# Optimization experiments

Hardware: AMD Instinct MI355X
Metric: run time of the kernel (lower is better)

Reference implementation:

```python
import jax, jax.numpy as jnp
import numpy as np
from jax import lax

B, N, G, K, D = 16, 8192, 512, 32, 128
MLP = [128, 128, 256]
EPS = 1e-5


def setup_inputs() -> dict:
    key = jax.random.key(0)
    ks = jax.random.split(key, 2 + len(MLP))
    inp = {
        "xyz": jax.random.normal(ks[0], (B, N, 3), jnp.float32),
        "points": jax.random.normal(ks[1], (B, N, D), jnp.float32),
    }
    last = D
    for li, oc in enumerate(MLP, 1):
        inp[f"W{li}"] = jax.random.normal(ks[1 + li], (oc, last), jnp.float32) / np.float32(np.sqrt(last))
        inp[f"b{li}"] = jnp.zeros((oc,), jnp.float32)
        inp[f"g{li}"] = jnp.ones((oc,), jnp.float32)
        inp[f"be{li}"] = jnp.zeros((oc,), jnp.float32)
        last = oc
    return inp


def _fps(xyz, num_group):
    # farthest point sampling, deterministic start at index 0 -> idx [B, G]
    b, n, _ = xyz.shape
    init_idx = jnp.zeros((b,), jnp.int32)

    def step(carry, _):
        dists, last_idx = carry                                   # [B,N], [B]
        last = jnp.take_along_axis(xyz, last_idx[:, None, None], axis=1)  # [B,1,3]
        d = jnp.sum((xyz - last) ** 2, axis=-1)                   # [B,N]
        dists = jnp.minimum(dists, d)
        nxt = jnp.argmax(dists, axis=1).astype(jnp.int32)
        return (dists, nxt), nxt

    init = (jnp.full((b, n), 1e10, jnp.float32), init_idx)
    _, rest = lax.scan(step, init, None, length=num_group - 1)    # [G-1, B]
    return jnp.concatenate([init_idx[None, :], rest], axis=0).T   # [B, G]


def _forward(xyz, points, layers):
    b = xyz.shape[0]
    center_idx = _fps(xyz, G)                                       # [B,G]
    center = jnp.take_along_axis(xyz, center_idx[:, :, None], axis=1)  # [B,G,3]
    # KNN: pairwise squared distances center->points, top-k smallest
    d2 = (jnp.sum(center ** 2, -1)[:, :, None]
          + jnp.sum(xyz ** 2, -1)[:, None, :]
          - 2.0 * jnp.einsum("bgc,bnc->bgn", center, xyz))          # [B,G,N]
    _, idx = lax.top_k(-d2, K)                                      # [B,G,K]
    feats = jnp.take_along_axis(points, idx.reshape(b, G * K, 1), axis=1)
    feats = feats.reshape(b, G, K, -1)                              # [B,G,K,D]
    x = feats.transpose(0, 3, 2, 1)                                 # [B,D,K,G]
    for (W, bb, g, be) in layers:
        x = jnp.einsum("oc,bckg->bokg", W, x) + bb[None, :, None, None]
        m = jnp.mean(x, axis=(0, 2, 3), keepdims=True)
        v = jnp.var(x, axis=(0, 2, 3), keepdims=True)               # biased, as torch BN
        x = (x - m) * lax.rsqrt(v + EPS) * g[None, :, None, None] + be[None, :, None, None]
        x = jax.nn.relu(x)
    new_points = jnp.max(x, axis=2).transpose(0, 2, 1)              # [B,G,C_out]
    return center, new_points


def reference(xyz, points, W1, b1, g1, be1, W2, b2, g2, be2, W3, b3, g3, be3):
    layers = [(W1, b1, g1, be1), (W2, b2, g2, be2), (W3, b3, g3, be3)]
    return _forward(xyz, points, layers)
```

## Files before the change

kernel.cpp:

```cpp
#include <hip/hip_runtime.h>
#include <hip/hip_bf16.h>

#define BB 16
#define NN 8192
#define GG 512
#define KK 32
#define DD 128

typedef __attribute__((ext_vector_type(8))) short bf16x8;
typedef __attribute__((ext_vector_type(4))) float f32x4;
typedef __attribute__((ext_vector_type(2))) float f32x2;
typedef __attribute__((ext_vector_type(2))) unsigned int u32x2;
typedef __attribute__((ext_vector_type(4))) unsigned int u32x4;
typedef __attribute__((ext_vector_type(2))) unsigned long long u64x2;

__device__ __forceinline__ unsigned short f2bf(float f){
  unsigned int u = __builtin_bit_cast(unsigned int, f);
  unsigned int r = (u + 0x7FFFu + ((u >> 16) & 1u)) >> 16;
  return (unsigned short)r;
}
__device__ __forceinline__ float bf2f(unsigned short h){
  unsigned int u = ((unsigned int)h) << 16;
  return __builtin_bit_cast(float, u);
}
// ... 110 lines not shown
#undef RESCAN2
      bv = gmin[0]; bi = gidx[0];
#pragma unroll
      for (int gi = 1; gi < 8; ++gi)
        if (gmin[gi] < bv){ bv = gmin[gi]; bi = gidx[gi]; }
    }
  }

  if (lane < KK) wlist[w][lane] = mykey;
  __syncthreads();
  if (lane < KK){
    unsigned long long K = mykey;
    const unsigned long long* other = wlist[1 - w];
    int cnt = 0;
#pragma unroll
    for (int j = 0; j < KK; ++j) cnt += (other[j] < K) ? 1 : 0;
    int rank = lane + cnt;
    if (rank < KK) outidx[rank] = (int)(unsigned int)K;
  }
  __syncthreads();
  if (t128 < KK) kidx[(size_t)bg*KK + t128] = outidx[t128];
}

__global__ __launch_bounds__(1024)
void fps_a_kernel(const float* __restrict__ xyz, const float* __restrict__ points,
                  const float* __restrict__ W1, const float* __restrict__ W2,
                  const float* __restrict__ W3,
                  float* __restrict__ center_out, float* __restrict__ ddws,
                  float* __restrict__ xs, float* __restrict__ ys,
                  float* __restrict__ zs, float* __restrict__ pps,
                  unsigned short* __restrict__ Wbf,
                  unsigned short* __restrict__ pointsbf)
{
#pragma clang fp contract(off)
  __shared__ unsigned long long slot[3][2] __attribute__((aligned(16)));
  __shared__ float tbl[NN][4] __attribute__((aligned(16)));
  __shared__ float outbuf[GG][4] __attribute__((aligned(16)));
  int t = threadIdx.x;
  if (blockIdx.x >= BB){
    int pb = blockIdx.x - BB;
    size_t i = ((size_t)pb*1024 + t)*8;
    f32x4 u0 = *(const f32x4*)(points + i);
    f32x4 u1 = *(const f32x4*)(points + i + 4);
    unsigned int w0 = f2bf(u0[0]) | ((unsigned int)f2bf(u0[1]) << 16);
    unsigned int w1 = f2bf(u0[2]) | ((unsigned int)f2bf(u0[3]) << 16);
    unsigned int w2 = f2bf(u1[0]) | ((unsigned int)f2bf(u1[1]) << 16);
    unsigned int w3 = f2bf(u1[2]) | ((unsigned int)f2bf(u1[3]) << 16);
    u32x4 pv = {w0, w1, w2, w3};
    *(u32x4*)(pointsbf + i) = pv;
    if (pb < 128){
      int n = pb*1024 + t;
      float x = xyz[(size_t)n*3 + 0];
      float y = xyz[(size_t)n*3 + 1];
      float z = xyz[(size_t)n*3 + 2];
      xs[n] = x; ys[n] = y; zs[n] = z;
      pps[n] = (x*x + y*y) + z*z;
    }
    if (pb < 64){
      int n = pb*1024 + t;
      float v;
      if (n < 16384)      v = W1[n];
      else if (n < 32768) v = W2[n - 16384];
      else                v = W3[n - 32768];
      Wbf[n] = f2bf(v);
    }
    return;
  }
  int b = blockIdx.x;
  int lane = t & 63, wid = t >> 6;
  const float* base = xyz + (size_t)b * NN * 3;
  f32x2 px[4], py[4], pz[4], dd[4];
#pragma unroll
  for (int i = 0; i < 4; ++i){
    int n0 = i*2048 + t, n1 = n0 + 1024;
    float x0 = base[n0*3+0], y0 = base[n0*3+1], z0 = base[n0*3+2];
    float x1 = base[n1*3+0], y1 = base[n1*3+1], z1 = base[n1*3+2];
    px[i] = (f32x2){x0, x1}; py[i] = (f32x2){y0, y1}; pz[i] = (f32x2){z0, z1};
    dd[i] = (f32x2){1e10f, 1e10f};
    f32x4 c0 = {x0, y0, z0, 0.f}, c1 = {x1, y1, z1, 0.f};
    *(f32x4*)&tbl[n0][0] = c0;
    *(f32x4*)&tbl[n1][0] = c1;
  }
  float lx = base[0], ly = base[1], lz = base[2];
  if (t < 6) slot[t >> 1][t & 1] = 0;
  if (t == 0){
    f32x4 ob = {lx, ly, lz, 0.f};
    *(f32x4*)&outbuf[0][0] = ob;
  }
  __syncthreads();
  for (int g = 1; g < 256; ++g){
    f32x2 lxv = (f32x2){lx, lx}, lyv = (f32x2){ly, ly}, lzv = (f32x2){lz, lz};
    f32x2 vm = (f32x2){-1.f, -1.f};
#pragma unroll
    for (int i = 0; i < 4; ++i){
      f32x2 dx = px[i] - lxv, dy = py[i] - lyv, dz = pz[i] - lzv;
      f32x2 s = (dx*dx + dy*dy) + dz*dz;
      f32x2 nd = __builtin_elementwise_min(dd[i], s);
      dd[i] = nd;
      vm = __builtin_elementwise_max(vm, nd);
    }
    float m = fmaxf(vm.x, vm.y);
    int mi = 0x7FFFFFFF;
#pragma unroll
    for (int i = 3; i >= 0; --i){
      int n0 = i*2048 + t;
      if (dd[i].y == m) mi = n0 + 1024;
      if (dd[i].x == m) mi = n0;
    }
    float wmax = wave_max_f32(m);
    bool cnd = (m == wmax);
    unsigned long long mask = __ballot(cnd);
    int n_wave;
    if (__popcll(mask) == 1){
      n_wave = __builtin_amdgcn_readlane(mi, (int)__builtin_ctzll(mask));
    } else {
      int cand = cnd ? mi : 0x7FFFFFFF;
      n_wave = wave_min_i32(cand);
    }
    unsigned long long key =
        ((unsigned long long)__builtin_bit_cast(unsigned int, wmax) << 32)
      | (unsigned int)(~n_wave);
    int p = g - (g/3)*3;
    if (lane == 0) atomicMax(&slot[p][wid & 1], key);
    __syncthreads();
    u64x2 sA = *(const u64x2*)&slot[p][0];
    unsigned long long M = sA.x > sA.y ? sA.x : sA.y;
    int n_win = (int)~((unsigned int)M);
    f32x4 cw = *(const f32x4*)&tbl[n_win][0];
    lx = cw[0]; ly = cw[1]; lz = cw[2];
    if (t == 0) *(f32x4*)&outbuf[g][0] = cw;
    if (t < 2){
      int z = p + 2; if (z >= 3) z -= 3;
      slot[z][t] = 0;
    }
  }
  __syncthreads();
  if (t < 256){
    center_out[((size_t)b*GG + t)*3 + 0] = outbuf[t][0];
    center_out[((size_t)b*GG + t)*3 + 1] = outbuf[t][1];
    center_out[((size_t)b*GG + t)*3 + 2] = outbuf[t][2];
  }
  f32x4 s0 = {dd[0].x, dd[0].y, dd[1].x, dd[1].y};
  f32x4 s1 = {dd[2].x, dd[2].y, dd[3].x, dd[3].y};
  float* dp = ddws + ((size_t)b*1024 + t)*8;
  *(f32x4*)dp       = s0;
  *(f32x4*)(dp + 4) = s1;
}

__global__ __launch_bounds__(1024)
void fps_b_kernel(const float* __restrict__ xyz, float* __restrict__ center_out,
                  const float* __restrict__ ddws,
                  const float* __restrict__ xs, const float* __restrict__ ys,
                  const float* __restrict__ zs, const float* __restrict__ pps,
                  int* __restrict__ kidx)
{
#pragma clang fp contract(off)
  __shared__ unsigned long long slot[3][2] __attribute__((aligned(16)));
  __shared__ float tbl[NN][4] __attribute__((aligned(16)));
  __shared__ float outbuf[GG][4] __attribute__((aligned(16)));
  __shared__ unsigned long long kwl[8][2][KK] __attribute__((aligned(16)));
  __shared__ int kout[8][KK];
  int t = threadIdx.x;
  if (blockIdx.x >= BB){
    int pb = blockIdx.x - BB;
    int sub = t >> 7, t128 = t & 127;
    int idx = pb*8 + sub;
    int b = idx >> 8, g = idx & 255;
    knn_group(b*GG + g, t128, xs, ys, zs, pps, center_out, kidx,
              kwl[sub], kout[sub]);
    return;
  }
  int b = blockIdx.x;
  int lane = t & 63, wid = t >> 6;
  const float* base = xyz + (size_t)b * NN * 3;
  f32x2 px[4], py[4], pz[4], dd[4];
  const float* dp = ddws + ((size_t)b*1024 + t)*8;
  f32x4 s0 = *(const f32x4*)dp;
  f32x4 s1 = *(const f32x4*)(dp + 4);
  dd[0] = (f32x2){s0[0], s0[1]};
  dd[1] = (f32x2){s0[2], s0[3]};
  dd[2] = (f32x2){s1[0], s1[1]};
  dd[3] = (f32x2){s1[2], s1[3]};
#pragma unroll
  for (int i = 0; i < 4; ++i){
    int n0 = i*2048 + t, n1 = n0 + 1024;
    float x0 = base[n0*3+0], y0 = base[n0*3+1], z0 = base[n0*3+2];
    float x1 = base[n1*3+0], y1 = base[n1*3+1], z1 = base[n1*3+2];
    px[i] = (f32x2){x0, x1}; py[i] = (f32x2){y0, y1}; pz[i] = (f32x2){z0, z1};
    f32x4 c0 = {x0, y0, z0, 0.f}, c1 = {x1, y1, z1, 0.f};
    *(f32x4*)&tbl[n0][0] = c0;
    *(f32x4*)&tbl[n1][0] = c1;
  }
  float lx = center_out[((size_t)b*GG + 255)*3 + 0];
  float ly = center_out[((size_t)b*GG + 255)*3 + 1];
  float lz = center_out[((size_t)b*GG + 255)*3 + 2];
  if (t < 6) slot[t >> 1][t & 1] = 0;
  __syncthreads();
  for (int g = 256; g < GG; ++g){
    f32x2 lxv = (f32x2){lx, lx}, lyv = (f32x2){ly, ly}, lzv = (f32x2){lz, lz};
    f32x2 vm = (f32x2){-1.f, -1.f};
#pragma unroll
    for (int i = 0; i < 4; ++i){
      f32x2 dx = px[i] - lxv, dy = py[i] - lyv, dz = pz[i] - lzv;
      f32x2 s = (dx*dx + dy*dy) + dz*dz;
      f32x2 nd = __builtin_elementwise_min(dd[i], s);
      dd[i] = nd;
      vm = __builtin_elementwise_max(vm, nd);
    }
    float m = fmaxf(vm.x, vm.y);
    int mi = 0x7FFFFFFF;
#pragma unroll
    for (int i = 3; i >= 0; --i){
      int n0 = i*2048 + t;
      if (dd[i].y == m) mi = n0 + 1024;
      if (dd[i].x == m) mi = n0;
    }
    float wmax = wave_max_f32(m);
    bool cnd = (m == wmax);
    unsigned long long mask = __ballot(cnd);
    int n_wave;
    if (__popcll(mask) == 1){
      n_wave = __builtin_amdgcn_readlane(mi, (int)__builtin_ctzll(mask));
    } else {
      int cand = cnd ? mi : 0x7FFFFFFF;
      n_wave = wave_min_i32(cand);
    }
    unsigned long long key =
        ((unsigned long long)__builtin_bit_cast(unsigned int, wmax) << 32)
      | (unsigned int)(~n_wave);
    int p = g - (g/3)*3;
    if (lane == 0) atomicMax(&slot[p][wid & 1], key);
    __syncthreads();
    u64x2 sA = *(const u64x2*)&slot[p][0];
    unsigned long long M = sA.x > sA.y ? sA.x : sA.y;
    int n_win = (int)~((unsigned int)M);
    f32x4 cw = *(const f32x4*)&tbl[n_win][0];
    lx = cw[0]; ly = cw[1]; lz = cw[2];
    if (t == 0) *(f32x4*)&outbuf[g][0] = cw;
    if (t < 2){
      int z = p + 2; if (z >= 3) z -= 3;
      slot[z][t] = 0;
    }
  }
  __syncthreads();
  if (t < 256){
    int g = 256 + t;
    center_out[((size_t)b*GG + g)*3 + 0] = outbuf[g][0];
    center_out[((size_t)b*GG + g)*3 + 1] = outbuf[g][1];
    center_out[((size_t)b*GG + g)*3 + 2] = outbuf[g][2];
  }
}

template<int OC, int MODE, bool STATS, bool STORE, bool POOL>
__device__ __forceinline__ void gemm_body(int sbid, int t, int slot,
    const unsigned short* __restrict__ Wbf, const float* __restrict__ bias,
    const unsigned short* __restrict__ pointsbf, const int* __restrict__ kidx,
    const unsigned short* __restrict__ Xin,
    const float* __restrict__ psum_in, const float* __restrict__ gin,
    const float* __restrict__ bein,
    unsigned short* __restrict__ Yout, float* __restrict__ psum,
    float* __restrict__ rawmax, float* __restrict__ rawmin,
    unsigned short* smem, float* ssc, float* ssh)
{
  constexpr int MF = OC / 64;
  int l = t & 63, w = t >> 6;
  int l15 = l & 15, lh = l >> 4;
  int jbase = sbid * 64;
  int obase = w * (OC / 4);

  if constexpr (MODE == 1){
    if (t < 128){
      float s = 0.f, q = 0.f;
#pragma unroll
      for (int sl = 0; sl < 64; ++sl){
        s += psum_in[sl*128 + t];
        q += psum_in[64*128 + sl*128 + t];
      }
      const float inv = 1.f / 262144.f;
      float mean = s * inv;
      float var  = q * inv - mean*mean;
      float sc = gin[t] * rsqrtf(var + 1e-5f);
      ssc[t] = sc;
      ssh[t] = bein[t] - mean*sc;
    }
  }

  bf16x8 a[MF][4];
#pragma unroll
  for (int m = 0; m < MF; ++m)
#pragma unroll
    for (int kf = 0; kf < 4; ++kf){
      int row = obase + m*16 + l15;
      int c8  = kf*32 + lh*8;
      a[m][kf] = *(const bf16x8*)(Wbf + (size_t)row*128 + c8);
    }

  if constexpr (MODE == 1) __syncthreads();

#pragma unroll
  for (int q = 0; q < 4; ++q){
    int ci = q*256 + t;
    int j = ci >> 4, cc = ci & 15;
    unsigned short* dst = &smem[j*128 + ((cc ^ (j & 15)) * 8)];
    if constexpr (MODE == 0){
      int jg = jbase + j;
      int bb = jg >> 14;
      int row = kidx[jg];
      const unsigned short* src = pointsbf + ((size_t)bb*NN + row)*DD + cc*8;
      *(u32x4*)dst = *(const u32x4*)src;
    } else {
      const unsigned short* src = Xin + ((size_t)(jbase + j))*128 + cc*8;
      u32x4 v = *(const u32x4*)src;
      int c0 = cc * 8;
      unsigned int wo[4];
#pragma unroll
      for (int p = 0; p < 4; ++p){
        float x0 = bf2f((unsigned short)(v[p] & 0xFFFFu));
        float x1 = bf2f((unsigned short)(v[p] >> 16));
        x0 = fmaxf(fmaf(x0, ssc[c0 + 2*p],     ssh[c0 + 2*p]),     0.f);
        x1 = fmaxf(fmaf(x1, ssc[c0 + 2*p + 1], ssh[c0 + 2*p + 1]), 0.f);
        wo[p] = f2bf(x0) | ((unsigned int)f2bf(x1) << 16);
      }
      u32x4 pv = {wo[0], wo[1], wo[2], wo[3]};
      *(u32x4*)dst = pv;
    }
  }
  __syncthreads();

  f32x4 acc[MF][4];
#pragma unroll
  for (int m = 0; m < MF; ++m)
#pragma unroll
    for (int n = 0; n < 4; ++n)
      acc[m][n] = (f32x4){0.f, 0.f, 0.f, 0.f};

#pragma unroll
  for (int n = 0; n < 4; ++n){
    bf16x8 bfr[4];
    int j = n*16 + l15;
#pragma unroll
    for (int kf = 0; kf < 4; ++kf){
      int ch = kf*4 + lh;
      bfr[kf] = *(const bf16x8*)&smem[j*128 + ((ch ^ (j & 15)) * 8)];
    }
#pragma unroll
    for (int m = 0; m < MF; ++m)
#pragma unroll
      for (int kf = 0; kf < 4; ++kf)
        acc[m][n] = __builtin_amdgcn_mfma_f32_16x16x32_bf16(a[m][kf], bfr[kf], acc[m][n], 0, 0, 0);
  }

#pragma unroll
  for (int m = 0; m < MF; ++m){
    int o0 = obase + m*16 + lh*4;
    f32x4 bv = *(const f32x4*)(bias + o0);
#pragma unroll
    for (int n = 0; n < 4; ++n) acc[m][n] += bv;
  }

  if constexpr (STATS){
#pragma unroll
    for (int m = 0; m < MF; ++m){
#pragma unroll
      for (int r = 0; r < 4; ++r){
        float s = 0.f, q2 = 0.f;
#pragma unroll
        for (int n = 0; n < 4; ++n){ float v = acc[m][n][r]; s += v; q2 += v*v; }
        s  += __shfl_xor(s, 1);  s  += __shfl_xor(s, 2);  s  += __shfl_xor(s, 4);  s  += __shfl_xor(s, 8);
        q2 += __shfl_xor(q2, 1); q2 += __shfl_xor(q2, 2); q2 += __shfl_xor(q2, 4); q2 += __shfl_xor(q2, 8);
        if (l15 == 0){
          int o = obase + m*16 + lh*4 + r;
          atomicAdd(psum + slot*OC + o, s);
          atomicAdd(psum + 64*OC + slot*OC + o, q2);
        }
      }
    }
  }

  if constexpr (POOL){
#pragma unroll
    for (int m = 0; m < MF; ++m){
      int o0 = obase + m*16 + lh*4;
      f32x4 gmx0, gmx1, gmn0, gmn1;
#pragma unroll
      for (int r = 0; r < 4; ++r){
        float v0 = acc[m][0][r], v1 = acc[m][1][r];
        float v2 = acc[m][2][r], v3 = acc[m][3][r];
        float ax0 = fmaxf(v0, v1), ax1 = fmaxf(v2, v3);
        float an0 = fminf(v0, v1), an1 = fminf(v2, v3);
#pragma unroll
        for (int mk = 1; mk < 16; mk <<= 1){
          ax0 = fmaxf(ax0, __shfl_xor(ax0, mk));
          ax1 = fmaxf(ax1, __shfl_xor(ax1, mk));
          an0 = fminf(an0, __shfl_xor(an0, mk));
          an1 = fminf(an1, __shfl_xor(an1, mk));
        }
        gmx0[r] = ax0; gmx1[r] = ax1; gmn0[r] = an0; gmn1[r] = an1;
      }
      if (l15 == 0){
        int gg = jbase >> 5;
        *(f32x4*)(rawmax + (size_t)gg*256 + o0)       = gmx0;
        *(f32x4*)(rawmax + (size_t)(gg + 1)*256 + o0) = gmx1;
        *(f32x4*)(rawmin + (size_t)gg*256 + o0)       = gmn0;
        *(f32x4*)(rawmin + (size_t)(gg + 1)*256 + o0) = gmn1;
      }
    }
  }

  if constexpr (STORE){
    __syncthreads();
#pragma unroll
    for (int m = 0; m < MF; ++m){
      int o0 = obase + m*16 + lh*4;
      int co = o0 >> 2;
#pragma unroll
      for (int n = 0; n < 4; ++n){
        int j = n*16 + l15;
        unsigned int w0 = f2bf(acc[m][n][0]) | ((unsigned int)f2bf(acc[m][n][1]) << 16);
        unsigned int w1 = f2bf(acc[m][n][2]) | ((unsigned int)f2bf(acc[m][n][3]) << 16);
        u32x2 pv = {w0, w1};
        *(u32x2*)&smem[j*OC + ((co ^ ((j & 15) << 1)) * 4)] = pv;
      }
    }
    __syncthreads();
    constexpr int CPR = OC / 4;
    constexpr int CPT = (64 * CPR) / 256;
#pragma unroll
    for (int q = 0; q < CPT; ++q){
      int ci = q*256 + t;
      int j = ci / CPR, co = ci % CPR;
      u32x2 v = *(const u32x2*)&smem[j*OC + ((co ^ ((j & 15) << 1)) * 4)];
      *(u32x2*)(Yout + (size_t)(jbase + j)*OC + co*4) = v;
    }
  }
}

__global__ __launch_bounds__(256)
void knn_gemm1_kernel(const float* __restrict__ xs, const float* __restrict__ ys,
                      const float* __restrict__ zs, const float* __restrict__ pps,
                      const float* __restrict__ center, int* __restrict__ kidx,
                      const unsigned short* __restrict__ Wbf,
                      const float* __restrict__ b1,
                      const unsigned short* __restrict__ pointsbf,
                      unsigned short* __restrict__ Y1, float* __restrict__ psumA)
{
  __shared__ unsigned short smem[64 * 128];
  __shared__ unsigned long long kwl[2][2][KK] __attribute__((aligned(16)));
  __shared__ int kout[2][KK];
  int bid = blockIdx.x, t = threadIdx.x;
  if (bid < 2048){
    int swz = (bid & 7) * 256 + (bid >> 3);
    int sub = t >> 7, t128 = t & 127;
    int idx = swz*2 + sub;
    int b = idx >> 8, g = 256 + (idx & 255);
    knn_group(b*GG + g, t128, xs, ys, zs, pps, center, kidx,
              kwl[sub], kout[sub]);
    return;
  }
  int h = bid - 2048;
  int hs = (h & 7) * 256 + (h >> 3);
  int sbid = (hs >> 7) * 256 + (hs & 127);
  gemm_body<128, 0, true, true, false>(sbid, t, bid & 63,
      Wbf, b1, pointsbf, kidx, nullptr, nullptr, nullptr, nullptr,
      Y1, psumA, nullptr, nullptr, smem, nullptr, nullptr);
}

template<int OC, int MODE, bool STATS, bool STORE, bool POOL>
__global__ __launch_bounds__(256)
void gemm_kernel(int gridmode,
                 const unsigned short* __restrict__ Wbf, const float* __restrict__ bias,
                 const unsigned short* __restrict__ pointsbf, const int* __restrict__ kidx,
                 const unsigned short* __restrict__ Xin,
                 const float* __restrict__ psum_in, const float* __restrict__ gin,
                 const float* __restrict__ bein,
                 unsigned short* __restrict__ Yout, float* __restrict__ psum,
                 float* __restrict__ rawmax, float* __restrict__ rawmin)
{
  __shared__ unsigned short smem[64 * OC];
  __shared__ float ssc[128], ssh[128];
  int bid = blockIdx.x, t = threadIdx.x;
  int sbid;
  if (gridmode == 0){
    sbid = (bid & 7) * 512 + (bid >> 3);
  } else {
    int hs = (bid & 7) * 256 + (bid >> 3);
    sbid = (hs >> 7) * 256 + 128 + (hs & 127);
  }
  gemm_body<OC, MODE, STATS, STORE, POOL>(sbid, t, bid & 63,
      Wbf, bias, pointsbf, kidx, Xin, psum_in, gin, bein,
      Yout, psum, rawmax, rawmin, smem, ssc, ssh);
}

__global__ __launch_bounds__(256)
void finish3_kernel(const float* __restrict__ psumC, const float* __restrict__ g3,
                    const float* __restrict__ be3, const float* __restrict__ rawmax,
                    const float* __restrict__ rawmin, float* __restrict__ opool)
{
  __shared__ float ssc[256], ssh[256];
  int t = threadIdx.x;
  {
    float s = 0.f, q = 0.f;
#pragma unroll
    for (int sl = 0; sl < 64; ++sl){
      s += psumC[sl*256 + t];
      q += psumC[64*256 + sl*256 + t];
    }
    const float inv = 1.f / 262144.f;
    float mean = s * inv;
    float var  = q * inv - mean*mean;
    float sc = g3[t] * rsqrtf(var + 1e-5f);
    ssc[t] = sc;
    ssh[t] = be3[t] - mean*sc;
// ... 37 lines not shown
  auto alloc = [&](size_t bytes) -> void* {
    void* p = ws + off;
    off += (bytes + 255) & ~(size_t)255;
    return p;
  };
  unsigned short* Y1   = (unsigned short*)alloc((size_t)262144*128*2);
  unsigned short* Y2   = (unsigned short*)alloc((size_t)262144*128*2);
  int*   kidx = (int*)  alloc((size_t)262144*4);
  unsigned short* Wbf = (unsigned short*)alloc((size_t)65536*2);
  float* rawmax = (float*)alloc((size_t)8192*256*4);
  float* rawmin = (float*)alloc((size_t)8192*256*4);
  float* psumA = (float*)alloc((size_t)2*64*128*4);
  float* psumB = (float*)alloc((size_t)2*64*128*4);
  float* psumC = (float*)alloc((size_t)2*64*256*4);
  float* xsb  = (float*)alloc((size_t)131072*4);
  float* ysb  = (float*)alloc((size_t)131072*4);
  float* zsb  = (float*)alloc((size_t)131072*4);
  float* ppsb = (float*)alloc((size_t)131072*4);
  float* ddws = (float*)alloc((size_t)16*1024*8*4);
  unsigned short* pointsbf = Y2;

  hipMemsetAsync(psumA, 0, (size_t)(2*64*128 + 2*64*128 + 2*64*256)*4 + 1024, stream);

  fps_a_kernel<<<BB + 2048, 1024, 0, stream>>>(
      xyz, points, W1, W2, W3, center, ddws, xsb, ysb, zsb, ppsb, Wbf, pointsbf);
  fps_b_kernel<<<BB + 512, 1024, 0, stream>>>(
      xyz, center, ddws, xsb, ysb, zsb, ppsb, kidx);

  knn_gemm1_kernel<<<4096, 256, 0, stream>>>(
      xsb, ysb, zsb, ppsb, center, kidx, Wbf, b1, pointsbf, Y1, psumA);

  gemm_kernel<128, 0, true, true, false><<<2048, 256, 0, stream>>>(
      2, Wbf, b1, pointsbf, kidx, nullptr, nullptr, nullptr, nullptr,
      Y1, psumA, nullptr, nullptr);

  gemm_kernel<128, 1, true, true, false><<<4096, 256, 0, stream>>>(
      0, Wbf + 16384, b2, nullptr, nullptr, Y1, psumA, g1, be1,
      Y2, psumB, nullptr, nullptr);

  gemm_kernel<256, 1, true, false, true><<<4096, 256, 0, stream>>>(
      0, Wbf + 32768, b3, nullptr, nullptr, Y2, psumB, g2, be2,
      nullptr, psumC, rawmax, rawmin);

  finish3_kernel<<<512, 256, 0, stream>>>(psumC, g3, be3, rawmax, rawmin, opool);
}
```

Baseline: 779.3 us.

## Split FPS into four phases and overlap KNN and GEMM1 with each phase

The serial farthest-point-sampling loop is now split into four launches of 128 centers each instead of two of 256. Filler blocks in each launch run KNN for the centers from the previous phase and layer-1 GEMM tiles for centers from two phases back. The aim is to hide more of the latency-bound FPS chain behind independent work and shrink the tail kernels. In exchange it adds two kernel launches and reloads the point coordinates and distance state for each phase. Co-resident filler blocks may also contend with the FPS blocks for CU resources.

```diff
diff --git a/kernel.cpp b/kernel.cpp
--- a/kernel.cpp
+++ b/kernel.cpp
@@ -156,22 +156,327 @@
   if (t128 < KK) kidx[(size_t)bg*KK + t128] = outidx[t128];
 }
 
+__device__ __forceinline__ void fps_part(const float* __restrict__ xyz,
+    float* __restrict__ center_out, float* __restrict__ ddws,
+    int b, int t, int g0, int g1, bool save_dd, char* lds)
+{
+#pragma clang fp contract(off)
+  float (*tbl)[4]    = (float(*)[4])lds;
+  float (*outbuf)[4] = (float(*)[4])(lds + 131072);
+  unsigned long long (*slot)[2] =
+      (unsigned long long(*)[2])(lds + 131072 + 2048);
+  int lane = t & 63, wid = t >> 6;
+  const float* base = xyz + (size_t)b * NN * 3;
+  f32x2 px[4], py[4], pz[4], dd[4];
+  if (g0 == 1){
+#pragma unroll
+    for (int i = 0; i < 4; ++i) dd[i] = (f32x2){1e10f, 1e10f};
+  } else {
+    const float* dp = ddws + ((size_t)b*1024 + t)*8;
+    f32x4 s0 = *(const f32x4*)dp;
+    f32x4 s1 = *(const f32x4*)(dp + 4);
+    dd[0] = (f32x2){s0[0], s0[1]};
+    dd[1] = (f32x2){s0[2], s0[3]};
+    dd[2] = (f32x2){s1[0], s1[1]};
+    dd[3] = (f32x2){s1[2], s1[3]};
+  }
+#pragma unroll
+  for (int i = 0; i < 4; ++i){
+    int n0 = i*2048 + t, n1 = n0 + 1024;
+    float x0 = base[n0*3+0], y0 = base[n0*3+1], z0 = base[n0*3+2];
+    float x1 = base[n1*3+0], y1 = base[n1*3+1], z1 = base[n1*3+2];
+    px[i] = (f32x2){x0, x1}; py[i] = (f32x2){y0, y1}; pz[i] = (f32x2){z0, z1};
+    f32x4 c0 = {x0, y0, z0, 0.f}, c1 = {x1, y1, z1, 0.f};
+    *(f32x4*)&tbl[n0][0] = c0;
+    *(f32x4*)&tbl[n1][0] = c1;
+  }
+  float lx, ly, lz;
+  if (g0 == 1){ lx = base[0]; ly = base[1]; lz = base[2]; }
+  else {
+    lx = center_out[((size_t)b*GG + g0 - 1)*3 + 0];
+    ly = center_out[((size_t)b*GG + g0 - 1)*3 + 1];
+    lz = center_out[((size_t)b*GG + g0 - 1)*3 + 2];
+  }
+  if (t < 6) slot[t >> 1][t & 1] = 0;
+  __syncthreads();
+  for (int g = g0; g < g1; ++g){
+    f32x2 lxv = (f32x2){lx, lx}, lyv = (f32x2){ly, ly}, lzv = (f32x2){lz, lz};
+    f32x2 vm = (f32x2){-1.f, -1.f};
+#pragma unroll
+    for (int i = 0; i < 4; ++i){
+      f32x2 dx = px[i] - lxv, dy = py[i] - lyv, dz = pz[i] - lzv;
+      f32x2 s = (dx*dx + dy*dy) + dz*dz;
+      f32x2 nd = __builtin_elementwise_min(dd[i], s);
+      dd[i] = nd;
+      vm = __builtin_elementwise_max(vm, nd);
+    }
+    float m = fmaxf(vm.x, vm.y);
+    int mi = 0x7FFFFFFF;
+#pragma unroll
+    for (int i = 3; i >= 0; --i){
+      int n0 = i*2048 + t;
+      if (dd[i].y == m) mi = n0 + 1024;
+      if (dd[i].x == m) mi = n0;
+    }
+    float wmax = wave_max_f32(m);
+    bool cnd = (m == wmax);
+    unsigned long long mask = __ballot(cnd);
+    int n_wave;
+    if (__popcll(mask) == 1){
+      n_wave = __builtin_amdgcn_readlane(mi, (int)__builtin_ctzll(mask));
+    } else {
+      int cand = cnd ? mi : 0x7FFFFFFF;
+      n_wave = wave_min_i32(cand);
+    }
+    unsigned long long key =
+        ((unsigned long long)__builtin_bit_cast(unsigned int, wmax) << 32)
+      | (unsigned int)(~n_wave);
+    int p = g - (g/3)*3;
+    if (lane == 0) atomicMax(&slot[p][wid & 1], key);
+    __syncthreads();
+    u64x2 sA = *(const u64x2*)&slot[p][0];
+    unsigned long long M = sA.x > sA.y ? sA.x : sA.y;
+    int n_win = (int)~((unsigned int)M);
+    f32x4 cw = *(const f32x4*)&tbl[n_win][0];
+    lx = cw[0]; ly = cw[1]; lz = cw[2];
+    if (t == 0) *(f32x4*)&outbuf[g - g0][0] = cw;
+    if (t < 2){
+      int z = p + 2; if (z >= 3) z -= 3;
+      slot[z][t] = 0;
+    }
+  }
+  __syncthreads();
+  if (t < g1 - g0){
+    int g = g0 + t;
+    center_out[((size_t)b*GG + g)*3 + 0] = outbuf[t][0];
+    center_out[((size_t)b*GG + g)*3 + 1] = outbuf[t][1];
+    center_out[((size_t)b*GG + g)*3 + 2] = outbuf[t][2];
+  }
+  if (g0 == 1 && t == 0){
+    center_out[((size_t)b*GG)*3 + 0] = base[0];
+    center_out[((size_t)b*GG)*3 + 1] = base[1];
+    center_out[((size_t)b*GG)*3 + 2] = base[2];
+  }
+  if (save_dd){
+    f32x4 s0 = {dd[0].x, dd[0].y, dd[1].x, dd[1].y};
+    f32x4 s1 = {dd[2].x, dd[2].y, dd[3].x, dd[3].y};
+    float* dp = ddws + ((size_t)b*1024 + t)*8;
+    *(f32x4*)dp       = s0;
+    *(f32x4*)(dp + 4) = s1;
+  }
+}
+
+template<int OC, int MODE, bool STATS, bool STORE, bool POOL>
+__device__ __forceinline__ void gemm_body(int sbid, int t,
+    const unsigned short* __restrict__ Wbf, const float* __restrict__ bias,
+    const unsigned short* __restrict__ pointsbf, const int* __restrict__ kidx,
+    const unsigned short* __restrict__ Xin,
+    const float* __restrict__ psum_in, const float* __restrict__ gin,
+    const float* __restrict__ bein,
+    unsigned short* __restrict__ Yout, float* __restrict__ psum,
+    float* __restrict__ rawmax, float* __restrict__ rawmin,
+    unsigned short* smem, float* ssc, float* ssh)
+{
+  constexpr int MF = OC / 64;
+  int l = t & 63, w = t >> 6;
+  int l15 = l & 15, lh = l >> 4;
+  int jbase = sbid * 64;
+  int obase = w * (OC / 4);
+  int slot = sbid & 63;
+
+  if constexpr (MODE == 1){
+    if (t < 128){
+      float s = 0.f, q = 0.f;
+#pragma unroll
+      for (int sl = 0; sl < 64; ++sl){
+        s += psum_in[sl*128 + t];
+        q += psum_in[64*128 + sl*128 + t];
+      }
+      const float inv = 1.f / 262144.f;
+      float mean = s * inv;
+      float var  = q * inv - mean*mean;
+      float sc = gin[t] * rsqrtf(var + 1e-5f);
+      ssc[t] = sc;
+      ssh[t] = bein[t] - mean*sc;
+    }
+  }
+
+  bf16x8 a[MF][4];
+#pragma unroll
+  for (int m = 0; m < MF; ++m)
+#pragma unroll
+    for (int kf = 0; kf < 4; ++kf){
+      int row = obase + m*16 + l15;
+      int c8  = kf*32 + lh*8;
+      a[m][kf] = *(const bf16x8*)(Wbf + (size_t)row*128 + c8);
+    }
+
+  if constexpr (MODE == 1) __syncthreads();
+
+#pragma unroll
+  for (int q = 0; q < 4; ++q){
+    int ci = q*256 + t;
+    int j = ci >> 4, cc = ci & 15;
+    unsigned short* dst = &smem[j*128 + ((cc ^ (j & 15)) * 8)];
+    if constexpr (MODE == 0){
+      int jg = jbase + j;
+      int bb = jg >> 14;
+      int row = kidx[jg];
+      const unsigned short* src = pointsbf + ((size_t)bb*NN + row)*DD + cc*8;
+      *(u32x4*)dst = *(const u32x4*)src;
+    } else {
+      const unsigned short* src = Xin + ((size_t)(jbase + j))*128 + cc*8;
+      u32x4 v = *(const u32x4*)src;
+      int c0 = cc * 8;
+      unsigned int wo[4];
+#pragma unroll
+      for (int p = 0; p < 4; ++p){
+        float x0 = bf2f((unsigned short)(v[p] & 0xFFFFu));
+        float x1 = bf2f((unsigned short)(v[p] >> 16));
+        x0 = fmaxf(fmaf(x0, ssc[c0 + 2*p],     ssh[c0 + 2*p]),     0.f);
+        x1 = fmaxf(fmaf(x1, ssc[c0 + 2*p + 1], ssh[c0 + 2*p + 1]), 0.f);
+        wo[p] = f2bf(x0) | ((unsigned int)f2bf(x1) << 16);
+      }
+      u32x4 pv = {wo[0], wo[1], wo[2], wo[3]};
+      *(u32x4*)dst = pv;
+    }
+  }
+  __syncthreads();
+
+  f32x4 acc[MF][4];
+#pragma unroll
+  for (int m = 0; m < MF; ++m)
+#pragma unroll
+    for (int n = 0; n < 4; ++n)
+      acc[m][n] = (f32x4){0.f, 0.f, 0.f, 0.f};
+
+#pragma unroll
+  for (int n = 0; n < 4; ++n){
+    bf16x8 bfr[4];
+    int j = n*16 + l15;
+#pragma unroll
+    for (int kf = 0; kf < 4; ++kf){
+      int ch = kf*4 + lh;
+      bfr[kf] = *(const bf16x8*)&smem[j*128 + ((ch ^ (j & 15)) * 8)];
+    }
+#pragma unroll
+    for (int m = 0; m < MF; ++m)
+#pragma unroll
+      for (int kf = 0; kf < 4; ++kf)
+        acc[m][n] = __builtin_amdgcn_mfma_f32_16x16x32_bf16(a[m][kf], bfr[kf], acc[m][n], 0, 0, 0);
+  }
+
+#pragma unroll
+  for (int m = 0; m < MF; ++m){
+    int o0 = obase + m*16 + lh*4;
+    f32x4 bv = *(const f32x4*)(bias + o0);
+#pragma unroll
+    for (int n = 0; n < 4; ++n) acc[m][n] += bv;
+  }
+
+  if constexpr (STATS){
+#pragma unroll
+    for (int m = 0; m < MF; ++m){
+#pragma unroll
+      for (int r = 0; r < 4; ++r){
+        float s = 0.f, q2 = 0.f;
+#pragma unroll
+        for (int n = 0; n < 4; ++n){ float v = acc[m][n][r]; s += v; q2 += v*v; }
+        s  += __shfl_xor(s, 1);  s  += __shfl_xor(s, 2);  s  += __shfl_xor(s, 4);  s  += __shfl_xor(s, 8);
+        q2 += __shfl_xor(q2, 1); q2 += __shfl_xor(q2, 2); q2 += __shfl_xor(q2, 4); q2 += __shfl_xor(q2, 8);
+        if (l15 == 0){
+          int o = obase + m*16 + lh*4 + r;
+          atomicAdd(psum + slot*OC + o, s);
+          atomicAdd(psum + 64*OC + slot*OC + o, q2);
+        }
+      }
+    }
+  }
+
+  if constexpr (POOL){
+#pragma unroll
+    for (int m = 0; m < MF; ++m){
+      int o0 = obase + m*16 + lh*4;
+      f32x4 gmx0, gmx1, gmn0, gmn1;
+#pragma unroll
+      for (int r = 0; r < 4; ++r){
+        float v0 = acc[m][0][r], v1 = acc[m][1][r];
+        float v2 = acc[m][2][r], v3 = acc[m][3][r];
+        float ax0 = fmaxf(v0, v1), ax1 = fmaxf(v2, v3);
+        float an0 = fminf(v0, v1), an1 = fminf(v2, v3);
+#pragma unroll
+        for (int mk = 1; mk < 16; mk <<= 1){
+          ax0 = fmaxf(ax0, __shfl_xor(ax0, mk));
+          ax1 = fmaxf(ax1, __shfl_xor(ax1, mk));
+          an0 = fminf(an0, __shfl_xor(an0, mk));
+          an1 = fminf(an1, __shfl_xor(an1, mk));
+        }
+        gmx0[r] = ax0; gmx1[r] = ax1; gmn0[r] = an0; gmn1[r] = an1;
+      }
+      if (l15 == 0){
+        int gg = jbase >> 5;
+        *(f32x4*)(rawmax + (size_t)gg*256 + o0)       = gmx0;
+        *(f32x4*)(rawmax + (size_t)(gg + 1)*256 + o0) = gmx1;
+        *(f32x4*)(rawmin + (size_t)gg*256 + o0)       = gmn0;
+        *(f32x4*)(rawmin + (size_t)(gg + 1)*256 + o0) = gmn1;
+      }
+    }
+  }
+
+  if constexpr (STORE){
+    __syncthreads();
+#pragma unroll
+    for (int m = 0; m < MF; ++m){
+      int o0 = obase + m*16 + lh*4;
+      int co = o0 >> 2;
+#pragma unroll
+      for (int n = 0; n < 4; ++n){
+        int j = n*16 + l15;
+        unsigned int w0 = f2bf(acc[m][n][0]) | ((unsigned int)f2bf(acc[m][n][1]) << 16);
+        unsigned int w1 = f2bf(acc[m][n][2]) | ((unsigned int)f2bf(acc[m][n][3]) << 16);
+        u32x2 pv = {w0, w1};
+        *(u32x2*)&smem[j*OC + ((co ^ ((j & 15) << 1)) * 4)] = pv;
+      }
+    }
+    __syncthreads();
+    constexpr int CPR = OC / 4;
+    constexpr int CPT = (64 * CPR) / 256;
+#pragma unroll
+    for (int q = 0; q < CPT; ++q){
+      int ci = q*256 + t;
+      int j = ci / CPR, co = ci % CPR;
+      u32x2 v = *(const u32x2*)&smem[j*OC + ((co ^ ((j & 15) << 1)) * 4)];
+      *(u32x2*)(Yout + (size_t)(jbase + j)*OC + co*4) = v;
+    }
+  }
+}
+
+#define LDSB (131072 + 2048 + 64)
+
+template<int PH>
 __global__ __launch_bounds__(1024)
-void fps_a_kernel(const float* __restrict__ xyz, const float* __restrict__ points,
-                  const float* __restrict__ W1, const float* __restrict__ W2,
-                  const float* __restrict__ W3,
-                  float* __restrict__ center_out, float* __restrict__ ddws,
-                  float* __restrict__ xs, float* __restrict__ ys,
-                  float* __restrict__ zs, float* __restrict__ pps,
-                  unsigned short* __restrict__ Wbf,
-                  unsigned short* __restrict__ pointsbf)
-{
+void fps_phase(const float* __restrict__ xyz, const float* __restrict__ points,
+               const float* __restrict__ W1, const float* __restrict__ W2,
+               const float* __restrict__ W3,
+               float* __restrict__ center_out, float* __restrict__ ddws,
+               float* __restrict__ xs, float* __restrict__ ys,
+               float* __restrict__ zs, float* __restrict__ pps,
+               unsigned short* __restrict__ Wbf,
+               unsigned short* __restrict__ pointsbf,
+               int* __restrict__ kidx,
+               const float* __restrict__ b1,
+               unsigned short* __restrict__ Y1, float* __restrict__ psumA)
+{
+  __shared__ __attribute__((aligned(16))) char lds[LDSB];
+  int t = threadIdx.x;
+  if (blockIdx.x < BB){
+    constexpr int g0 = (PH == 0) ? 1 : PH*128;
+    constexpr int g1 = (PH + 1)*128;
+    fps_part(xyz, center_out, ddws, blockIdx.x, t, g0, g1, PH < 3, lds);
+    return;
+  }
+  if constexpr (PH == 0){
 #pragma clang fp contract(off)
-  __shared__ unsigned long long slot[3][2] __attribute__((aligned(16)));
-  __shared__ float tbl[NN][4] __attribute__((aligned(16)));
-  __shared__ float outbuf[GG][4] __attribute__((aligned(16)));
-  int t = threadIdx.x;
-  if (blockIdx.x >= BB){
     int pb = blockIdx.x - BB;
     size_t i = ((size_t)pb*1024 + t)*8;
     f32x4 u0 = *(const f32x4*)(points + i);
@@ -198,412 +503,79 @@
       else                v = W3[n - 32768];
       Wbf[n] = f2bf(v);
     }
-    return;
-  }
-  int b = blockIdx.x;
-  int lane = t & 63, wid = t >> 6;
-  const float* base = xyz + (size_t)b * NN * 3;
-  f32x2 px[4], py[4], pz[4], dd[4];
-#pragma unroll
-  for (int i = 0; i < 4; ++i){
-    int n0 = i*2048 + t, n1 = n0 + 1024;
-    float x0 = base[n0*3+0], y0 = base[n0*3+1], z0 = base[n0*3+2];
-    float x1 = base[n1*3+0], y1 = base[n1*3+1], z1 = base[n1*3+2];
-    px[i] = (f32x2){x0, x1}; py[i] = (f32x2){y0, y1}; pz[i] = (f32x2){z0, z1};
-    dd[i] = (f32x2){1e10f, 1e10f};
-    f32x4 c0 = {x0, y0, z0, 0.f}, c1 = {x1, y1, z1, 0.f};
-    *(f32x4*)&tbl[n0][0] = c0;
-    *(f32x4*)&tbl[n1][0] = c1;
-  }
-  float lx = base[0], ly = base[1], lz = base[2];
-  if (t < 6) slot[t >> 1][t & 1] = 0;
-  if (t == 0){
-    f32x4 ob = {lx, ly, lz, 0.f};
-    *(f32x4*)&outbuf[0][0] = ob;
-  }
-  __syncthreads();
-  for (int g = 1; g < 256; ++g){
-    f32x2 lxv = (f32x2){lx, lx}, lyv = (f32x2){ly, ly}, lzv = (f32x2){lz, lz};
-    f32x2 vm = (f32x2){-1.f, -1.f};
-#pragma unroll
-    for (int i = 0; i < 4; ++i){
-      f32x2 dx = px[i] - lxv, dy = py[i] - lyv, dz = pz[i] - lzv;
-      f32x2 s = (dx*dx + dy*dy) + dz*dz;
-      f32x2 nd = __builtin_elementwise_min(dd[i], s);
-      dd[i] = nd;
-      vm = __builtin_elementwise_max(vm, nd);
-    }
-    float m = fmaxf(vm.x, vm.y);
-    int mi = 0x7FFFFFFF;
-#pragma unroll
-    for (int i = 3; i >= 0; --i){
-      int n0 = i*2048 + t;
-      if (dd[i].y == m) mi = n0 + 1024;
-      if (dd[i].x == m) mi = n0;
-    }
-    float wmax = wave_max_f32(m);
-    bool cnd = (m == wmax);
-    unsigned long long mask = __ballot(cnd);
-    int n_wave;
-    if (__popcll(mask) == 1){
-      n_wave = __builtin_amdgcn_readlane(mi, (int)__builtin_ctzll(mask));
-    } else {
-      int cand = cnd ? mi : 0x7FFFFFFF;
-      n_wave = wave_min_i32(cand);
-    }
-    unsigned long long key =
-        ((unsigned long long)__builtin_bit_cast(unsigned int, wmax) << 32)
-      | (unsigned int)(~n_wave);
-    int p = g - (g/3)*3;
-    if (lane == 0) atomicMax(&slot[p][wid & 1], key);
-    __syncthreads();
-    u64x2 sA = *(const u64x2*)&slot[p][0];
-    unsigned long long M = sA.x > sA.y ? sA.x : sA.y;
-    int n_win = (int)~((unsigned int)M);
-    f32x4 cw = *(const f32x4*)&tbl[n_win][0];
-    lx = cw[0]; ly = cw[1]; lz = cw[2];
-    if (t == 0) *(f32x4*)&outbuf[g][0] = cw;
-    if (t < 2){
-      int z = p + 2; if (z >= 3) z -= 3;
-      slot[z][t] = 0;
-    }
-  }
-  __syncthreads();
-  if (t < 256){
-    center_out[((size_t)b*GG + t)*3 + 0] = outbuf[t][0];
-    center_out[((size_t)b*GG + t)*3 + 1] = outbuf[t][1];
-    center_out[((size_t)b*GG + t)*3 + 2] = outbuf[t][2];
-  }
-  f32x4 s0 = {dd[0].x, dd[0].y, dd[1].x, dd[1].y};
-  f32x4 s1 = {dd[2].x, dd[2].y, dd[3].x, dd[3].y};
-  float* dp = ddws + ((size_t)b*1024 + t)*8;
-  *(f32x4*)dp       = s0;
-  *(f32x4*)(dp + 4) = s1;
-}
-
-__global__ __launch_bounds__(1024)
-void fps_b_kernel(const float* __restrict__ xyz, float* __restrict__ center_out,
-                  const float* __restrict__ ddws,
-                  const float* __restrict__ xs, const float* __restrict__ ys,
-                  const float* __restrict__ zs, const float* __restrict__ pps,
-                  int* __restrict__ kidx)
-{
-#pragma clang fp contract(off)
-  __shared__ unsigned long long slot[3][2] __attribute__((aligned(16)));
-  __shared__ float tbl[NN][4] __attribute__((aligned(16)));
-  __shared__ float outbuf[GG][4] __attribute__((aligned(16)));
-  __shared__ unsigned long long kwl[8][2][KK] __attribute__((aligned(16)));
-  __shared__ int kout[8][KK];
-  int t = threadIdx.x;
-  if (blockIdx.x >= BB){
+  } else {
     int pb = blockIdx.x - BB;
-    int sub = t >> 7, t128 = t & 127;
-    int idx = pb*8 + sub;
-    int b = idx >> 8, g = idx & 255;
-    knn_group(b*GG + g, t128, xs, ys, zs, pps, center_out, kidx,
-              kwl[sub], kout[sub]);
-    return;
-  }
-  int b = blockIdx.x;
-  int lane = t & 63, wid = t >> 6;
-  const float* base = xyz + (size_t)b * NN * 3;
-  f32x2 px[4], py[4], pz[4], dd[4];
-  const float* dp = ddws + ((size_t)b*1024 + t)*8;
-  f32x4 s0 = *(const f32x4*)dp;
-  f32x4 s1 = *(const f32x4*)(dp + 4);
-  dd[0] = (f32x2){s0[0], s0[1]};
-  dd[1] = (f32x2){s0[2], s0[3]};
-  dd[2] = (f32x2){s1[0], s1[1]};
-  dd[3] = (f32x2){s1[2], s1[3]};
-#pragma unroll
-  for (int i = 0; i < 4; ++i){
-    int n0 = i*2048 + t, n1 = n0 + 1024;
-    float x0 = base[n0*3+0], y0 = base[n0*3+1], z0 = base[n0*3+2];
-    float x1 = base[n1*3+0], y1 = base[n1*3+1], z1 = base[n1*3+2];
-    px[i] = (f32x2){x0, x1}; py[i] = (f32x2){y0, y1}; pz[i] = (f32x2){z0, z1};
-    f32x4 c0 = {x0, y0, z0, 0.f}, c1 = {x1, y1, z1, 0.f};
-    *(f32x4*)&tbl[n0][0] = c0;
-    *(f32x4*)&tbl[n1][0] = c1;
-  }
-  float lx = center_out[((size_t)b*GG + 255)*3 + 0];
-  float ly = center_out[((size_t)b*GG + 255)*3 + 1];
-  float lz = center_out[((size_t)b*GG + 255)*3 + 2];
-  if (t < 6) slot[t >> 1][t & 1] = 0;
-  __syncthreads();
-  for (int g = 256; g < GG; ++g){
-    f32x2 lxv = (f32x2){lx, lx}, lyv = (f32x2){ly, ly}, lzv = (f32x2){lz, lz};
-    f32x2 vm = (f32x2){-1.f, -1.f};
-#pragma unroll
-    for (int i = 0; i < 4; ++i){
-      f32x2 dx = px[i] - lxv, dy = py[i] - lyv, dz = pz[i] - lzv;
-      f32x2 s = (dx*dx + dy*dy) + dz*dz;
-      f32x2 nd = __builtin_elementwise_min(dd[i], s);
-      dd[i] = nd;
-      vm = __builtin_elementwise_max(vm, nd);
-    }
-    float m = fmaxf(vm.x, vm.y);
-    int mi = 0x7FFFFFFF;
-#pragma unroll
-    for (int i = 3; i >= 0; --i){
-      int n0 = i*2048 + t;
-      if (dd[i].y == m) mi = n0 + 1024;
-      if (dd[i].x == m) mi = n0;
-    }
-    float wmax = wave_max_f32(m);
-    bool cnd = (m == wmax);
-    unsigned long long mask = __ballot(cnd);
-    int n_wave;
-    if (__popcll(mask) == 1){
-      n_wave = __builtin_amdgcn_readlane(mi, (int)__builtin_ctzll(mask));
-    } else {
-      int cand = cnd ? mi : 0x7FFFFFFF;
-      n_wave = wave_min_i32(cand);
-    }
-    unsigned long long key =
-        ((unsigned long long)__builtin_bit_cast(unsigned int, wmax) << 32)
-      | (unsigned int)(~n_wave);
-    int p = g - (g/3)*3;
-    if (lane == 0) atomicMax(&slot[p][wid & 1], key);
-    __syncthreads();
-    u64x2 sA = *(const u64x2*)&slot[p][0];
-    unsigned long long M = sA.x > sA.y ? sA.x : sA.y;
-    int n_win = (int)~((unsigned int)M);
-    f32x4 cw = *(const f32x4*)&tbl[n_win][0];
-    lx = cw[0]; ly = cw[1]; lz = cw[2];
-    if (t == 0) *(f32x4*)&outbuf[g][0] = cw;
-    if (t < 2){
-      int z = p + 2; if (z >= 3) z -= 3;
-      slot[z][t] = 0;
-    }
-  }
-  __syncthreads();
-  if (t < 256){
-    int g = 256 + t;
-    center_out[((size_t)b*GG + g)*3 + 0] = outbuf[g][0];
-    center_out[((size_t)b*GG + g)*3 + 1] = outbuf[g][1];
-    center_out[((size_t)b*GG + g)*3 + 2] = outbuf[g][2];
-  }
-}
-
-template<int OC, int MODE, bool STATS, bool STORE, bool POOL>
-__device__ __forceinline__ void gemm_body(int sbid, int t, int slot,
-    const unsigned short* __restrict__ Wbf, const float* __restrict__ bias,
-    const unsigned short* __restrict__ pointsbf, const int* __restrict__ kidx,
-    const unsigned short* __restrict__ Xin,
-    const float* __restrict__ psum_in, const float* __restrict__ gin,
-    const float* __restrict__ bein,
-    unsigned short* __restrict__ Yout, float* __restrict__ psum,
-    float* __restrict__ rawmax, float* __restrict__ rawmin,
-    unsigned short* smem, float* ssc, float* ssh)
-{
-  constexpr int MF = OC / 64;
-  int l = t & 63, w = t >> 6;
-  int l15 = l & 15, lh = l >> 4;
-  int jbase = sbid * 64;
-  int obase = w * (OC / 4);
-
-  if constexpr (MODE == 1){
-    if (t < 128){
-      float s = 0.f, q = 0.f;
-#pragma unroll
-      for (int sl = 0; sl < 64; ++sl){
-        s += psum_in[sl*128 + t];
-        q += psum_in[64*128 + sl*128 + t];
-      }
-      const float inv = 1.f / 262144.f;
-      float mean = s * inv;
-      float var  = q * inv - mean*mean;
-      float sc = gin[t] * rsqrtf(var + 1e-5f);
-      ssc[t] = sc;
-      ssh[t] = bein[t] - mean*sc;
-    }
-  }
-
-  bf16x8 a[MF][4];
-#pragma unroll
-  for (int m = 0; m < MF; ++m)
-#pragma unroll
-    for (int kf = 0; kf < 4; ++kf){
-      int row = obase + m*16 + l15;
-      int c8  = kf*32 + lh*8;
-      a[m][kf] = *(const bf16x8*)(Wbf + (size_t)row*128 + c8);
-    }
-
-  if constexpr (MODE == 1) __syncthreads();
-
-#pragma unroll
-  for (int q = 0; q < 4; ++q){
-    int ci = q*256 + t;
-    int j = ci >> 4, cc = ci & 15;
-    unsigned short* dst = &smem[j*128 + ((cc ^ (j & 15)) * 8)];
-    if constexpr (MODE == 0){
-      int jg = jbase + j;
-      int bb = jg >> 14;
-      int row = kidx[jg];
-      const unsigned short* src = pointsbf + ((size_t)bb*NN + row)*DD + cc*8;
-      *(u32x4*)dst = *(const u32x4*)src;
-    } else {
-      const unsigned short* src = Xin + ((size_t)(jbase + j))*128 + cc*8;
-      u32x4 v = *(const u32x4*)src;
-      int c0 = cc * 8;
-      unsigned int wo[4];
-#pragma unroll
-      for (int p = 0; p < 4; ++p){
-        float x0 = bf2f((unsigned short)(v[p] & 0xFFFFu));
-        float x1 = bf2f((unsigned short)(v[p] >> 16));
-        x0 = fmaxf(fmaf(x0, ssc[c0 + 2*p],     ssh[c0 + 2*p]),     0.f);
-        x1 = fmaxf(fmaf(x1, ssc[c0 + 2*p + 1], ssh[c0 + 2*p + 1]), 0.f);
-        wo[p] = f2bf(x0) | ((unsigned int)f2bf(x1) << 16);
-      }
-      u32x4 pv = {wo[0], wo[1], wo[2], wo[3]};
-      *(u32x4*)dst = pv;
-    }
-  }
-  __syncthreads();
-
-  f32x4 acc[MF][4];
-#pragma unroll
-  for (int m = 0; m < MF; ++m)
-#pragma unroll
-    for (int n = 0; n < 4; ++n)
-      acc[m][n] = (f32x4){0.f, 0.f, 0.f, 0.f};
-
-#pragma unroll
-  for (int n = 0; n < 4; ++n){
-    bf16x8 bfr[4];
-    int j = n*16 + l15;
-#pragma unroll
-    for (int kf = 0; kf < 4; ++kf){
-      int ch = kf*4 + lh;
-      bfr[kf] = *(const bf16x8*)&smem[j*128 + ((ch ^ (j & 15)) * 8)];
-    }
-#pragma unroll
-    for (int m = 0; m < MF; ++m)
-#pragma unroll
-      for (int kf = 0; kf < 4; ++kf)
-        acc[m][n] = __builtin_amdgcn_mfma_f32_16x16x32_bf16(a[m][kf], bfr[kf], acc[m][n], 0, 0, 0);
-  }
-
-#pragma unroll
-  for (int m = 0; m < MF; ++m){
-    int o0 = obase + m*16 + lh*4;
-    f32x4 bv = *(const f32x4*)(bias + o0);
-#pragma unroll
-    for (int n = 0; n < 4; ++n) acc[m][n] += bv;
-  }
-
-  if constexpr (STATS){
-#pragma unroll
-    for (int m = 0; m < MF; ++m){
-#pragma unroll
-      for (int r = 0; r < 4; ++r){
-        float s = 0.f, q2 = 0.f;
-#pragma unroll
-        for (int n = 0; n < 4; ++n){ float v = acc[m][n][r]; s += v; q2 += v*v; }
-        s  += __shfl_xor(s, 1);  s  += __shfl_xor(s, 2);  s  += __shfl_xor(s, 4);  s  += __shfl_xor(s, 8);
-        q2 += __shfl_xor(q2, 1); q2 += __shfl_xor(q2, 2); q2 += __shfl_xor(q2, 4); q2 += __shfl_xor(q2, 8);
-        if (l15 == 0){
-          int o = obase + m*16 + lh*4 + r;
-          atomicAdd(psum + slot*OC + o, s);
-          atomicAdd(psum + 64*OC + slot*OC + o, q2);
-        }
-      }
-    }
-  }
-
-  if constexpr (POOL){
-#pragma unroll
-    for (int m = 0; m < MF; ++m){
-      int o0 = obase + m*16 + lh*4;
-      f32x4 gmx0, gmx1, gmn0, gmn1;
-#pragma unroll
-      for (int r = 0; r < 4; ++r){
-        float v0 = acc[m][0][r], v1 = acc[m][1][r];
-        float v2 = acc[m][2][r], v3 = acc[m][3][r];
-        float ax0 = fmaxf(v0, v1), ax1 = fmaxf(v2, v3);
-        float an0 = fminf(v0, v1), an1 = fminf(v2, v3);
-#pragma unroll
-        for (int mk = 1; mk < 16; mk <<= 1){
-          ax0 = fmaxf(ax0, __shfl_xor(ax0, mk));
-          ax1 = fmaxf(ax1, __shfl_xor(ax1, mk));
-          an0 = fminf(an0, __shfl_xor(an0, mk));
-          an1 = fminf(an1, __shfl_xor(an1, mk));
-        }
-        gmx0[r] = ax0; gmx1[r] = ax1; gmn0[r] = an0; gmn1[r] = an1;
-      }
-      if (l15 == 0){
-        int gg = jbase >> 5;
-        *(f32x4*)(rawmax + (size_t)gg*256 + o0)       = gmx0;
-        *(f32x4*)(rawmax + (size_t)(gg + 1)*256 + o0) = gmx1;
-        *(f32x4*)(rawmin + (size_t)gg*256 + o0)       = gmn0;
-        *(f32x4*)(rawmin + (size_t)(gg + 1)*256 + o0) = gmn1;
-      }
-    }
-  }
-
-  if constexpr (STORE){
-    __syncthreads();
-#pragma unroll
-    for (int m = 0; m < MF; ++m){
-      int o0 = obase + m*16 + lh*4;
-      int co = o0 >> 2;
-#pragma unroll
-      for (int n = 0; n < 4; ++n){
-        int j = n*16 + l15;
-        unsigned int w0 = f2bf(acc[m][n][0]) | ((unsigned int)f2bf(acc[m][n][1]) << 16);
-        unsigned int w1 = f2bf(acc[m][n][2]) | ((unsigned int)f2bf(acc[m][n][3]) << 16);
-        u32x2 pv = {w0, w1};
-        *(u32x2*)&smem[j*OC + ((co ^ ((j & 15) << 1)) * 4)] = pv;
-      }
-    }
-    __syncthreads();
-    constexpr int CPR = OC / 4;
-    constexpr int CPT = (64 * CPR) / 256;
-#pragma unroll
-    for (int q = 0; q < CPT; ++q){
-      int ci = q*256 + t;
-      int j = ci / CPR, co = ci % CPR;
-      u32x2 v = *(const u32x2*)&smem[j*OC + ((co ^ ((j & 15) << 1)) * 4)];
-      *(u32x2*)(Yout + (size_t)(jbase + j)*OC + co*4) = v;
+    if (pb < 256){
+      unsigned long long (*kwl)[2][KK] = (unsigned long long(*)[2][KK])lds;
+      int* kout = (int*)(lds + 8*2*KK*8);
+      int sub = t >> 7, t128 = t & 127;
+      int idx = pb*8 + sub;
+      int b = idx >> 7, g = (PH-1)*128 + (idx & 127);
+      knn_group(b*GG + g, t128, xs, ys, zs, pps, center_out, kidx,
+                &kwl[sub][0], kout + sub*KK);
+    } else if constexpr (PH >= 2){
+      int hb = pb - 256;
+      int sub = t >> 8, t256 = t & 255;
+      int u = hb*4 + sub;
+      int us = (u & 7) * 128 + (u >> 3);
+      int b = us >> 6, tau = (PH-2)*64 + (us & 63);
+      int sbid = b*256 + tau;
+      unsigned short* smem = (unsigned short*)(lds + sub*16384);
+      gemm_body<128, 0, true, true, false>(sbid, t256,
+          Wbf, b1, pointsbf, kidx, nullptr, nullptr, nullptr, nullptr,
+          Y1, psumA, nullptr, nullptr, smem, nullptr, nullptr);
     }
   }
 }
 
 __global__ __launch_bounds__(256)
-void knn_gemm1_kernel(const float* __restrict__ xs, const float* __restrict__ ys,
-                      const float* __restrict__ zs, const float* __restrict__ pps,
-                      const float* __restrict__ center, int* __restrict__ kidx,
-                      const unsigned short* __restrict__ Wbf,
-                      const float* __restrict__ b1,
-                      const unsigned short* __restrict__ pointsbf,
-                      unsigned short* __restrict__ Y1, float* __restrict__ psumA)
+void knn_gemm_tail(const float* __restrict__ xs, const float* __restrict__ ys,
+                   const float* __restrict__ zs, const float* __restrict__ pps,
+                   const float* __restrict__ center, int* __restrict__ kidx,
+                   const unsigned short* __restrict__ Wbf,
+                   const float* __restrict__ b1,
+                   const unsigned short* __restrict__ pointsbf,
+                   unsigned short* __restrict__ Y1, float* __restrict__ psumA)
 {
   __shared__ unsigned short smem[64 * 128];
   __shared__ unsigned long long kwl[2][2][KK] __attribute__((aligned(16)));
   __shared__ int kout[2][KK];
   int bid = blockIdx.x, t = threadIdx.x;
-  if (bid < 2048){
-    int swz = (bid & 7) * 256 + (bid >> 3);
+  if (bid < 1024){
+    int swz = (bid & 7) * 128 + (bid >> 3);
     int sub = t >> 7, t128 = t & 127;
     int idx = swz*2 + sub;
-    int b = idx >> 8, g = 256 + (idx & 255);
+    int b = idx >> 7, g = 384 + (idx & 127);
     knn_group(b*GG + g, t128, xs, ys, zs, pps, center, kidx,
               kwl[sub], kout[sub]);
     return;
   }
-  int h = bid - 2048;
-  int hs = (h & 7) * 256 + (h >> 3);
-  int sbid = (hs >> 7) * 256 + (hs & 127);
-  gemm_body<128, 0, true, true, false>(sbid, t, bid & 63,
+  int h = bid - 1024;
+  int hs = (h & 7) * 128 + (h >> 3);
+  int b = hs >> 6, tau = 128 + (hs & 63);
+  gemm_body<128, 0, true, true, false>(b*256 + tau, t,
       Wbf, b1, pointsbf, kidx, nullptr, nullptr, nullptr, nullptr,
       Y1, psumA, nullptr, nullptr, smem, nullptr, nullptr);
 }
 
+__global__ __launch_bounds__(256)
+void gemm1d_kernel(const unsigned short* __restrict__ Wbf, const float* __restrict__ b1,
+                   const unsigned short* __restrict__ pointsbf,
+                   const int* __restrict__ kidx,
+                   unsigned short* __restrict__ Y1, float* __restrict__ psumA)
+{
+  __shared__ unsigned short smem[64 * 128];
+  int bid = blockIdx.x, t = threadIdx.x;
+  int hs = (bid & 7) * 128 + (bid >> 3);
+  int b = hs >> 6, tau = 192 + (hs & 63);
+  gemm_body<128, 0, true, true, false>(b*256 + tau, t,
+      Wbf, b1, pointsbf, kidx, nullptr, nullptr, nullptr, nullptr,
+      Y1, psumA, nullptr, nullptr, smem, nullptr, nullptr);
+}
+
 template<int OC, int MODE, bool STATS, bool STORE, bool POOL>
 __global__ __launch_bounds__(256)
-void gemm_kernel(int gridmode,
-                 const unsigned short* __restrict__ Wbf, const float* __restrict__ bias,
-                 const unsigned short* __restrict__ pointsbf, const int* __restrict__ kidx,
+void gemm_kernel(const unsigned short* __restrict__ Wbf, const float* __restrict__ bias,
                  const unsigned short* __restrict__ Xin,
                  const float* __restrict__ psum_in, const float* __restrict__ gin,
                  const float* __restrict__ bein,
@@ -613,15 +585,9 @@
   __shared__ unsigned short smem[64 * OC];
   __shared__ float ssc[128], ssh[128];
   int bid = blockIdx.x, t = threadIdx.x;
-  int sbid;
-  if (gridmode == 0){
-    sbid = (bid & 7) * 512 + (bid >> 3);
-  } else {
-    int hs = (bid & 7) * 256 + (bid >> 3);
-    sbid = (hs >> 7) * 256 + 128 + (hs & 127);
-  }
-  gemm_body<OC, MODE, STATS, STORE, POOL>(sbid, t, bid & 63,
-      Wbf, bias, pointsbf, kidx, Xin, psum_in, gin, bein,
+  int sbid = (bid & 7) * 512 + (bid >> 3);
+  gemm_body<OC, MODE, STATS, STORE, POOL>(sbid, t,
+      Wbf, bias, nullptr, nullptr, Xin, psum_in, gin, bein,
       Yout, psum, rawmax, rawmin, smem, ssc, ssh);
 }
 
@@ -705,25 +671,28 @@
 
   hipMemsetAsync(psumA, 0, (size_t)(2*64*128 + 2*64*128 + 2*64*256)*4 + 1024, stream);
 
-  fps_a_kernel<<<BB + 2048, 1024, 0, stream>>>(
-      xyz, points, W1, W2, W3, center, ddws, xsb, ysb, zsb, ppsb, Wbf, pointsbf);
-  fps_b_kernel<<<BB + 512, 1024, 0, stream>>>(
-      xyz, center, ddws, xsb, ysb, zsb, ppsb, kidx);
-
-  knn_gemm1_kernel<<<4096, 256, 0, stream>>>(
+  fps_phase<0><<<BB + 2048, 1024, 0, stream>>>(
+      xyz, points, W1, W2, W3, center, ddws, xsb, ysb, zsb, ppsb,
+      Wbf, pointsbf, kidx, b1, Y1, psumA);
+  fps_phase<1><<<BB + 256, 1024, 0, stream>>>(
+      xyz, points, W1, W2, W3, center, ddws, xsb, ysb, zsb, ppsb,
+      Wbf, pointsbf, kidx, b1, Y1, psumA);
+  fps_phase<2><<<BB + 256 + 256, 1024, 0, stream>>>(
+      xyz, points, W1, W2, W3, center, ddws, xsb, ysb, zsb, ppsb,
+      Wbf, pointsbf, kidx, b1, Y1, psumA);
+  fps_phase<3><<<BB + 256 + 256, 1024, 0, stream>>>(
+      xyz, points, W1, W2, W3, center, ddws, xsb, ysb, zsb, ppsb,
+      Wbf, pointsbf, kidx, b1, Y1, psumA);
+
+  knn_gemm_tail<<<2048, 256, 0, stream>>>(
       xsb, ysb, zsb, ppsb, center, kidx, Wbf, b1, pointsbf, Y1, psumA);
-
-  gemm_kernel<128, 0, true, true, false><<<2048, 256, 0, stream>>>(
-      2, Wbf, b1, pointsbf, kidx, nullptr, nullptr, nullptr, nullptr,
-      Y1, psumA, nullptr, nullptr);
+  gemm1d_kernel<<<1024, 256, 0, stream>>>(Wbf, b1, pointsbf, kidx, Y1, psumA);
 
   gemm_kernel<128, 1, true, true, false><<<4096, 256, 0, stream>>>(
-      0, Wbf + 16384, b2, nullptr, nullptr, Y1, psumA, g1, be1,
-      Y2, psumB, nullptr, nullptr);
+      Wbf + 16384, b2, Y1, psumA, g1, be1, Y2, psumB, nullptr, nullptr);
 
   gemm_kernel<256, 1, true, false, true><<<4096, 256, 0, stream>>>(
-      0, Wbf + 32768, b3, nullptr, nullptr, Y2, psumB, g2, be2,
-      nullptr, psumC, rawmax, rawmin);
+      Wbf + 32768, b3, Y2, psumB, g2, be2, nullptr, psumC, rawmax, rawmin);
 
   finish3_kernel<<<512, 256, 0, stream>>>(psumC, g3, be3, rawmax, rawmin, opool);
 }
```

Result: faster. 725.4 us (-6.9%).
